# Kernel tuning notes

Hardware: AMD Instinct MI355X
Metric: run time of the kernel (lower is better)

The kernel has to match this reference:

```python
import jax, jax.numpy as jnp
import numpy as np


def _dF(field, c):
    """Central differences of component c of field [B,X,Y,Z,C] -> [B,X-2,Y-2,Z-2,3]."""
    f = field[..., c]
    dx = (f[:, 2:, 1:-1, 1:-1] - f[:, :-2, 1:-1, 1:-1]) * 0.5
    dy = (f[:, 1:-1, 2:, 1:-1] - f[:, 1:-1, :-2, 1:-1]) * 0.5
    dz = (f[:, 1:-1, 1:-1, 2:] - f[:, 1:-1, 1:-1, :-2]) * 0.5
    return jnp.stack((dx, dy, dz), axis=4)


def setup_inputs() -> dict:
    key = jax.random.key(0)
    grid = jax.random.normal(key, (2, 160, 160, 160, 3), dtype=jnp.float32)
    return {"grid": grid}


def reference(grid):
    # First derivatives of each displacement component: [B,X-2,Y-2,Z-2,3]
    dx = _dF(grid, 0)
    dy = _dF(grid, 1)
    dz = _dF(grid, 2)
    # Second derivatives: [B,X-4,Y-4,Z-4,3]
    dxx = _dF(dx, 0)
    dyy = _dF(dy, 1)
    dzz = _dF(dz, 2)
    dxy = _dF(dx, 1)
    dyz = _dF(dy, 2)
    dxz = _dF(dx, 2)
    penalty = jnp.sum(dxx ** 2 + dyy ** 2 + dzz ** 2
                      + 2.0 * (dxy ** 2 + dyz ** 2 + dxz ** 2))
    return penalty / dxx.size
```

## Files before the change

kernel.cpp:

```cpp
#include <hip/hip_runtime.h>

#define OY 480
#define OX 76800
#define SB 12288000
#define RST 212
#define SLICEF (16*RST)
#define IT 12
#define NSEG 13
#define NBLK 1014
#define INV_SIZE (1.0f/22778496.0f)

#define ROW_SHL1 0x101
#define ROW_SHL2 0x102
#define ROW_SHR1 0x111
#define ROW_SHR2 0x112

template<int CTRL>
__device__ __forceinline__ float dppf(float x){
    return __int_as_float(__builtin_amdgcn_update_dpp(
        0, __float_as_int(x), CTRL, 0xF, 0xF, true));
}

__device__ __forceinline__ float4 ld4p(const float* p){ return *reinterpret_cast<const float4*>(p); }
__device__ __forceinline__ void st4p(float* p, float4 v){ *reinterpret_cast<float4*>(p) = v; }

__device__ __forceinline__ void ld24(float* d, const float* p){
    float4 x0=ld4p(p), x1=ld4p(p+4), x2=ld4p(p+8), x3=ld4p(p+12), x4=ld4p(p+16), x5=ld4p(p+20);
    d[0]=x0.x; d[1]=x0.y; d[2]=x0.z; d[3]=x0.w;
    d[4]=x1.x; d[5]=x1.y; d[6]=x1.z; d[7]=x1.w;
    d[8]=x2.x; d[9]=x2.y; d[10]=x2.z; d[11]=x2.w;
    d[12]=x3.x; d[13]=x3.y; d[14]=x3.z; d[15]=x3.w;
    d[16]=x4.x; d[17]=x4.y; d[18]=x4.z; d[19]=x4.w;
    d[20]=x5.x; d[21]=x5.y; d[22]=x5.z; d[23]=x5.w;
}

#define STEP(P, V0a, V0b, DP) { \
    const int s = 2*d + (P); \
    const bool doLoad = (s <= 14); \
    float4 a0, a1, a2, a3; \
    if (doLoad) { \
        const float* bp = G + (size_t)(i0 - 1 + s) * OX; \
        a0 = ld4p(bp+gof0); a1 = ld4p(bp+gof1); a2 = ld4p(bp+gof2); a3 = ld4p(bp+gof3); \
    } \
    if (qact) { \
        const float* Lr = lds + (P)*SLICEF + oj; \
        float x[24]; ld24(x, Lr); \
        float dz0[4], dz1[4], dz2[4], dy0[4], dy1[4], v0c[4]; \
        _Pragma("unroll") for (int v=0; v<4; ++v) { \
            v0c[v] = x[3*v+6]; \
            dz0[v] = x[3*v+9]  - x[3*v+3]; \
            dz1[v] = x[3*v+10] - x[3*v+4]; \
            dz2[v] = x[3*v+11] - x[3*v+5]; \
            dy0[v] = dppf<ROW_SHR1>(x[3*v+6]) - dppf<ROW_SHL1>(x[3*v+6]); \
            dy1[v] = dppf<ROW_SHR1>(x[3*v+7]) - dppf<ROW_SHL1>(x[3*v+7]); \
        } \
        if (s >= 2 && s <= 13) { \
            _Pragma("unroll") for (int v=0; v<4; ++v) { \
                float c0 = x[3*v+6], c1 = x[3*v+7]; \
                float hy0 = dppf<ROW_SHR2>(c0) - 2.f*c0 + dppf<ROW_SHL2>(c0); \
                float hy1 = dppf<ROW_SHR2>(c1) - 2.f*c1 + dppf<ROW_SHL2>(c1); \
                float yz0 = dppf<ROW_SHR1>(dz0[v]) - dppf<ROW_SHL1>(dz0[v]); \
                float yz1 = dppf<ROW_SHR1>(dz1[v]) - dppf<ROW_SHL1>(dz1[v]); \
                float yz2 = dppf<ROW_SHR1>(dz2[v]) - dppf<ROW_SHL1>(dz2[v]); \
                if (vr) { \
                    float zz0 = x[3*v+12] - 2.f*x[3*v+6] + x[3*v]; \
                    float zz1 = x[3*v+13] - 2.f*x[3*v+7] + x[3*v+1]; \
                    float zz2 = x[3*v+14] - 2.f*x[3*v+8] + x[3*v+2]; \
                    cls2 = fmaf(zz0,zz0,cls2); cls2 = fmaf(zz1,zz1,cls2); cls1 = fmaf(zz2,zz2,cls1); \
                    cls2 = fmaf(hy0,hy0,cls2); cls1 = fmaf(hy1,hy1,cls1); \
                    cls4 = fmaf(yz0,yz0,cls4); cls3 = fmaf(yz1,yz1,cls3); cls1 = fmaf(yz2,yz2,cls1); \
                } \
            } \
        } \
        const bool eXY = vr && (s >= 3) && (s <= 14); \
        const bool eXX = vr && (s >= 4); \
        _Pragma("unroll") for (int v=0; v<4; ++v) { \
            if (eXY) { float h; \
                h = dy0[v] - DP[0][v]; cls3 = fmaf(h,h,cls3); \
                h = dy1[v] - DP[1][v]; cls1 = fmaf(h,h,cls1); \
                h = dz0[v] - DP[2][v]; cls3 = fmaf(h,h,cls3); \
                h = dz1[v] - DP[3][v]; cls2 = fmaf(h,h,cls2); \
                h = dz2[v] - DP[4][v]; cls1 = fmaf(h,h,cls1); \
            } \
            DP[0][v] = dy0[v]; DP[1][v] = dy1[v]; \
            DP[2][v] = dz0[v]; DP[3][v] = dz1[v]; DP[4][v] = dz2[v]; \
            if (eXX) { float h = v0c[v] - 2.f*V0a[v] + V0b[v]; cls1 = fmaf(h,h,cls1); } \
            V0b[v] = V0a[v]; V0a[v] = v0c[v]; \
        } \
    } \
    if (doLoad) { \
        float* Lw = lds + ((P)^1)*SLICEF; \
        if (wv0) st4p(Lw+lof0, a0); \
        if (wv1) st4p(Lw+lof1, a1); \
        if (wv2) st4p(Lw+lof2, a2); \
        if (wv3) st4p(Lw+lof3, a3); \
    } \
    __syncthreads(); \
}

__global__ __launch_bounds__(256)
void be_partials(const float* __restrict__ g, float* __restrict__ partial) {
    __shared__ float lds[2*SLICEF];
    __shared__ float wsum[4];

    const int tid = threadIdx.x;
    const int bid = blockIdx.x;
    const int is = bid % NSEG;
    int r1 = bid / NSEG;
    const int zt = r1 % 3;  r1 /= 3;
    const int jt = r1 % 13;
    const int bb = r1 / 13;

    const int j0  = 2 + jt*12;
    const int zlo = 64*zt;
    const int i0  = 2 + is*IT;
    const float* __restrict__ G = g + (size_t)bb*SB + (size_t)(j0-2)*OY + 3*zlo;

    const int vmaxq0 = (480 - 3*zlo) >> 2;
    const int vmaxq = vmaxq0 < 51 ? vmaxq0 : 51;
    int gof0,gof1,gof2,gof3, lof0,lof1,lof2,lof3;
    bool wv0,wv1,wv2,wv3;
    {
        int f, row, pos, vp;
        f = tid;       row = f/53; pos = f - 53*row; vp = pos < vmaxq ? pos : vmaxq-1;
        gof0 = row*OY + 4*vp; lof0 = row*RST + 4*pos; wv0 = pos < vmaxq;
        f = tid + 256; row = f/53; pos = f - 53*row; vp = pos < vmaxq ? pos : vmaxq-1;
        gof1 = row*OY + 4*vp; lof1 = row*RST + 4*pos; wv1 = pos < vmaxq;
        f = tid + 512; row = f/53; pos = f - 53*row; vp = pos < vmaxq ? pos : vmaxq-1;
        gof2 = row*OY + 4*vp; lof2 = row*RST + 4*pos; wv2 = pos < vmaxq;
        if (tid < 80) {
            f = tid + 768; row = f/53; pos = f - 53*row; vp = pos < vmaxq ? pos : vmaxq-1;
            gof3 = row*OY + 4*vp; lof3 = row*RST + 4*pos; wv3 = pos < vmaxq;
        } else { gof3 = 0; lof3 = 0; wv3 = false; }
    }

    const int r = tid & 15;
    const int Q = tid >> 4;
    const int qmax = (zt == 2) ? 7 : 16;
    const bool qact = Q < qmax;
    const bool vr = (r >= 2) && (r <= 13);
    const int oj = r*RST + 12*Q;

    float v0A0[4], v0A1[4], v0B0[4], v0B1[4];
    float dpA[5][4], dpB[5][4];
    #pragma unroll
    for (int v=0; v<4; ++v) {
        v0A0[v]=v0A1[v]=v0B0[v]=v0B1[v]=0.f;
        #pragma unroll
        for (int q=0; q<5; ++q) { dpA[q][v]=0.f; dpB[q][v]=0.f; }
    }
    float cls1=0.f, cls2=0.f, cls3=0.f, cls4=0.f;

    {
        const float* bp = G + (size_t)(i0-2)*OX;
        float4 a0=ld4p(bp+gof0), a1=ld4p(bp+gof1), a2=ld4p(bp+gof2), a3=ld4p(bp+gof3);
        if (wv0) st4p(lds+lof0, a0);
        if (wv1) st4p(lds+lof1, a1);
        if (wv2) st4p(lds+lof2, a2);
        if (wv3) st4p(lds+lof3, a3);
    }
    __syncthreads();

    #pragma unroll 1
    for (int d = 0; d < 8; ++d) {
        STEP(0, v0A0, v0A1, dpA)
        STEP(1, v0B0, v0B1, dpB)
    }

    float sv = fmaf(2.f, cls2, cls1);
    sv = fmaf(3.f, cls3, sv);
    sv = fmaf(4.f, cls4, sv);
    sv *= 0.0625f;

    #pragma unroll
    for (int off = 32; off > 0; off >>= 1) sv += __shfl_down(sv, off, 64);
    if ((tid & 63) == 0) wsum[tid >> 6] = sv;
    __syncthreads();
    if (tid == 0)
        partial[bid] = (wsum[0] + wsum[1]) + (wsum[2] + wsum[3]);
}

__global__ __launch_bounds__(256)
void be_final(const float* __restrict__ partial, float* __restrict__ out) {
    float s = 0.0f;
    for (int i = threadIdx.x; i < NBLK; i += 256) s += partial[i];
    #pragma unroll
    for (int off = 32; off > 0; off >>= 1) s += __shfl_down(s, off, 64);
    __shared__ float ws[4];
    if ((threadIdx.x & 63) == 0) ws[threadIdx.x >> 6] = s;
    __syncthreads();
    if (threadIdx.x == 0)
        out[0] = ((ws[0] + ws[1]) + (ws[2] + ws[3])) * INV_SIZE;
}

extern "C" void kernel_launch(void* const* d_in, const int* in_sizes, int n_in,
                              void* d_out, int out_size, void* d_ws, size_t ws_size,
                              hipStream_t stream) {
    const float* grid = (const float*)d_in[0];
    float* out = (float*)d_out;
    float* partials = (float*)d_ws;

    be_partials<<<dim3(NBLK), dim3(256), 0, stream>>>(grid, partials);
    be_final<<<1, 256, 0, stream>>>(partials, out);
}
```

Before: 152.4 us.

## Replace LDS slice staging with per-thread register double-buffered global loads

Removes the shared-memory double buffer and its per-step __syncthreads. Instead, each active thread loads its own 24-float window straight from global memory into registers, one x-slice ahead, alternating between two register buffers. This cuts the LDS store/load traffic and the block-wide barriers. In exchange, neighbouring threads' windows overlap, so global/L1 load traffic roughly doubles, the accesses are less coalesced, and register pressure rises.

After: 166.8 us. +9.4%, slower.

```diff
diff --git a/kernel.cpp b/kernel.cpp
--- a/kernel.cpp
+++ b/kernel.cpp
@@ -3,8 +3,6 @@
 #define OY 480
 #define OX 76800
 #define SB 12288000
-#define RST 212
-#define SLICEF (16*RST)
 #define IT 12
 #define NSEG 13
 #define NBLK 1014
@@ -22,29 +20,18 @@
 }
 
 __device__ __forceinline__ float4 ld4p(const float* p){ return *reinterpret_cast<const float4*>(p); }
-__device__ __forceinline__ void st4p(float* p, float4 v){ *reinterpret_cast<float4*>(p) = v; }
 
-__device__ __forceinline__ void ld24(float* d, const float* p){
-    float4 x0=ld4p(p), x1=ld4p(p+4), x2=ld4p(p+8), x3=ld4p(p+12), x4=ld4p(p+16), x5=ld4p(p+20);
-    d[0]=x0.x; d[1]=x0.y; d[2]=x0.z; d[3]=x0.w;
-    d[4]=x1.x; d[5]=x1.y; d[6]=x1.z; d[7]=x1.w;
-    d[8]=x2.x; d[9]=x2.y; d[10]=x2.z; d[11]=x2.w;
-    d[12]=x3.x; d[13]=x3.y; d[14]=x3.z; d[15]=x3.w;
-    d[16]=x4.x; d[17]=x4.y; d[18]=x4.z; d[19]=x4.w;
-    d[20]=x5.x; d[21]=x5.y; d[22]=x5.z; d[23]=x5.w;
-}
-
-#define STEP(P, V0a, V0b, DP) { \
+#define STEP(P, V0a, V0b, DP, WC, WN) { \
     const int s = 2*d + (P); \
-    const bool doLoad = (s <= 14); \
-    float4 a0, a1, a2, a3; \
-    if (doLoad) { \
-        const float* bp = G + (size_t)(i0 - 1 + s) * OX; \
-        a0 = ld4p(bp+gof0); a1 = ld4p(bp+gof1); a2 = ld4p(bp+gof2); a3 = ld4p(bp+gof3); \
-    } \
     if (qact) { \
-        const float* Lr = lds + (P)*SLICEF + oj; \
-        float x[24]; ld24(x, Lr); \
+        if (s <= 14) { \
+            WN[0]=ld4p(nx);    WN[1]=ld4p(nx+4);  WN[2]=ld4p(nx+8); \
+            WN[3]=ld4p(nx+12); WN[4]=ld4p(nx+16); WN[5]=ld4p(nx+20); \
+            nx += OX; \
+        } \
+        float x[24]; \
+        _Pragma("unroll") for (int q=0;q<6;++q){ \
+            x[4*q]=WC[q].x; x[4*q+1]=WC[q].y; x[4*q+2]=WC[q].z; x[4*q+3]=WC[q].w; } \
         float dz0[4], dz1[4], dz2[4], dy0[4], dy1[4], v0c[4]; \
         _Pragma("unroll") for (int v=0; v<4; ++v) { \
             v0c[v] = x[3*v+6]; \
@@ -88,19 +75,10 @@
             V0b[v] = V0a[v]; V0a[v] = v0c[v]; \
         } \
     } \
-    if (doLoad) { \
-        float* Lw = lds + ((P)^1)*SLICEF; \
-        if (wv0) st4p(Lw+lof0, a0); \
-        if (wv1) st4p(Lw+lof1, a1); \
-        if (wv2) st4p(Lw+lof2, a2); \
-        if (wv3) st4p(Lw+lof3, a3); \
-    } \
-    __syncthreads(); \
 }
 
 __global__ __launch_bounds__(256)
 void be_partials(const float* __restrict__ g, float* __restrict__ partial) {
-    __shared__ float lds[2*SLICEF];
     __shared__ float wsum[4];
 
     const int tid = threadIdx.x;
@@ -116,31 +94,15 @@
     const int i0  = 2 + is*IT;
     const float* __restrict__ G = g + (size_t)bb*SB + (size_t)(j0-2)*OY + 3*zlo;
 
-    const int vmaxq0 = (480 - 3*zlo) >> 2;
-    const int vmaxq = vmaxq0 < 51 ? vmaxq0 : 51;
-    int gof0,gof1,gof2,gof3, lof0,lof1,lof2,lof3;
-    bool wv0,wv1,wv2,wv3;
-    {
-        int f, row, pos, vp;
-        f = tid;       row = f/53; pos = f - 53*row; vp = pos < vmaxq ? pos : vmaxq-1;
-        gof0 = row*OY + 4*vp; lof0 = row*RST + 4*pos; wv0 = pos < vmaxq;
-        f = tid + 256; row = f/53; pos = f - 53*row; vp = pos < vmaxq ? pos : vmaxq-1;
-        gof1 = row*OY + 4*vp; lof1 = row*RST + 4*pos; wv1 = pos < vmaxq;
-        f = tid + 512; row = f/53; pos = f - 53*row; vp = pos < vmaxq ? pos : vmaxq-1;
-        gof2 = row*OY + 4*vp; lof2 = row*RST + 4*pos; wv2 = pos < vmaxq;
-        if (tid < 80) {
-            f = tid + 768; row = f/53; pos = f - 53*row; vp = pos < vmaxq ? pos : vmaxq-1;
-            gof3 = row*OY + 4*vp; lof3 = row*RST + 4*pos; wv3 = pos < vmaxq;
-        } else { gof3 = 0; lof3 = 0; wv3 = false; }
-    }
-
     const int r = tid & 15;
     const int Q = tid >> 4;
     const int qmax = (zt == 2) ? 7 : 16;
     const bool qact = Q < qmax;
     const bool vr = (r >= 2) && (r <= 13);
-    const int oj = r*RST + 12*Q;
+    const float* lane0 = G + (size_t)r*OY + 12*Q;
+    const float* nx = lane0 + (size_t)(i0-1)*OX;
 
+    float4 wA[6], wB[6];
     float v0A0[4], v0A1[4], v0B0[4], v0B1[4];
     float dpA[5][4], dpB[5][4];
     #pragma unroll
@@ -151,20 +113,16 @@
     }
     float cls1=0.f, cls2=0.f, cls3=0.f, cls4=0.f;
 
-    {
-        const float* bp = G + (size_t)(i0-2)*OX;
-        float4 a0=ld4p(bp+gof0), a1=ld4p(bp+gof1), a2=ld4p(bp+gof2), a3=ld4p(bp+gof3);
-        if (wv0) st4p(lds+lof0, a0);
-        if (wv1) st4p(lds+lof1, a1);
-        if (wv2) st4p(lds+lof2, a2);
-        if (wv3) st4p(lds+lof3, a3);
+    if (qact) {
+        const float* wp = lane0 + (size_t)(i0-2)*OX;
+        wA[0]=ld4p(wp);    wA[1]=ld4p(wp+4);  wA[2]=ld4p(wp+8);
+        wA[3]=ld4p(wp+12); wA[4]=ld4p(wp+16); wA[5]=ld4p(wp+20);
     }
-    __syncthreads();
 
     #pragma unroll 1
     for (int d = 0; d < 8; ++d) {
-        STEP(0, v0A0, v0A1, dpA)
-        STEP(1, v0B0, v0B1, dpB)
+        STEP(0, v0A0, v0A1, dpA, wA, wB)
+        STEP(1, v0B0, v0B1, dpB, wB, wA)
     }
 
     float sv = fmaf(2.f, cls2, cls1);
```
